# Kernel optimization log

Hardware: AMD Instinct MI355X
Metric: run time of the kernel (lower is better)

Reference implementation:

```python
import jax, jax.numpy as jnp
import numpy as np

B, NT, NC, EMB = 8, 512, 2048, 512
H, DK, DV = 8, 64, 64
EPS = 1e-6


def setup_inputs() -> dict:
    key = jax.random.key(0)
    ks = jax.random.split(key, 11)
    s = 1.0 / np.sqrt(EMB)
    return {
        "queries": jax.random.normal(ks[0], (B, NT, EMB), jnp.float32),
        "keys": jax.random.normal(ks[1], (B, NC, EMB), jnp.float32),
        "values": jax.random.normal(ks[2], (B, NC, EMB), jnp.float32),
        "W_At": jax.random.normal(ks[3], (H * DK, EMB), jnp.float32) * s,
        "b_At": jax.random.normal(ks[4], (H * DK,), jnp.float32) * s,
        "W_Ac": jax.random.normal(ks[5], (H * DK, EMB), jnp.float32) * s,
        "b_Ac": jax.random.normal(ks[6], (H * DK,), jnp.float32) * s,
        "W_Bc": jax.random.normal(ks[7], (H * DV, EMB), jnp.float32) * s,
        "b_Bc": jax.random.normal(ks[8], (H * DV,), jnp.float32) * s,
        "W_R": jax.random.normal(ks[9], (EMB, H * DV), jnp.float32) * (1.0 / np.sqrt(H * DV)),
        "b_R": jax.random.normal(ks[10], (EMB,), jnp.float32) * (1.0 / np.sqrt(H * DV)),
    }


def reference(queries, keys, values, W_At, b_At, W_Ac, b_Ac, W_Bc, b_Bc, W_R, b_R):
    b_s, n_t, _ = queries.shape
    n_c = keys.shape[1]
    # projections -> (b, h, n, d)
    q = (queries @ W_At.T + b_At).reshape(b_s, n_t, H, DK).transpose(0, 2, 1, 3)
    k = (keys @ W_Ac.T + b_Ac).reshape(b_s, n_c, H, DK).transpose(0, 2, 1, 3)
    v = (values @ W_Bc.T + b_Bc).reshape(b_s, n_c, H, DV).transpose(0, 2, 1, 3)
    # cosine similarity: q.k / max(||q||*||k||, eps) -- no (b,h,nt,nc,dk) broadcast
    dots = jnp.einsum("bhtd,bhcd->bhtc", q, k)
    qn = jnp.linalg.norm(q, axis=-1)  # (b,h,nt)
    kn = jnp.linalg.norm(k, axis=-1)  # (b,h,nc)
    denom = jnp.maximum(qn[..., :, None] * kn[..., None, :], EPS)
    att = jax.nn.softmax(dots / denom, axis=-1)
    out = jnp.einsum("bhtc,bhcd->bhtd", att, v)
    out = out.transpose(0, 2, 1, 3).reshape(b_s, n_t, H * DV)
    out = out @ W_R.T + b_R
    return (out, att)
```

## Files before the change

kernel.cpp:

```cpp
#include <hip/hip_runtime.h>

#define B_   8
#define NT_  512
#define NC_  2048
#define EMB_ 512
#define H_   8

typedef __attribute__((ext_vector_type(8))) short bf16x8;
typedef __attribute__((ext_vector_type(4))) float f32x4;

__device__ __forceinline__ unsigned short f2bf(float x) {
    unsigned u = __float_as_uint(x);
    u += 0x7fffu + ((u >> 16) & 1u);
    return (unsigned short)(u >> 16);
}
__device__ __forceinline__ float b2f(unsigned short h) {
    return __uint_as_float(((unsigned)h) << 16);
}

__device__ __forceinline__ int swz(int row, int col) {
    return row * 64 + ((((col >> 3) ^ row) & 7) << 3) + (col & 7);
}

__device__ __forceinline__ bf16x8 ldfrag(const unsigned short* t, int rowbase, int kq) {
    int lane = threadIdx.x & 63;
    int m = rowbase + (lane & 15);
    int k = kq + ((lane >> 4) << 3);
    return *(const bf16x8*)(t + swz(m, k));
}

template<int NCH>
__device__ __forceinline__ void stage_f32(unsigned short* tile, const float* src, int ld) {
    int tid = threadIdx.x;
#pragma unroll
    for (int i = 0; i < NCH; i++) {
        int ch  = tid + i * 256;
        int row = ch >> 3, c8 = ch & 7;
        const float4* p = (const float4*)(src + (size_t)row * ld + c8 * 8);
        float4 a = p[0], b = p[1];
        uint4 u;
        u.x = (unsigned)f2bf(a.x) | ((unsigned)f2bf(a.y) << 16);
        u.y = (unsigned)f2bf(a.z) | ((unsigned)f2bf(a.w) << 16);
        u.z = (unsigned)f2bf(b.x) | ((unsigned)f2bf(b.y) << 16);
        u.w = (unsigned)f2bf(b.z) | ((unsigned)f2bf(b.w) << 16);
        *(uint4*)(tile + row * 64 + (((c8 ^ row) & 7) << 3)) = u;
    }
}
template<int NCH>
__device__ __forceinline__ void stage_bf(unsigned short* tile, const unsigned short* src, int ld) {
    int tid = threadIdx.x;
#pragma unroll
    for (int i = 0; i < NCH; i++) {
        int ch  = tid + i * 256;
        int row = ch >> 3, c8 = ch & 7;
        uint4 u = *(const uint4*)(src + (size_t)row * ld + c8 * 8);
        *(uint4*)(tile + row * 64 + (((c8 ^ row) & 7) << 3)) = u;
    }
}

template<int MODE, bool ABF>
__global__ __launch_bounds__(256) void gemm512(const void* A, const float* W,
                                               const float* bias, void* dst, int sh)
{
    __shared__ unsigned short As[64 * 64];
    __shared__ unsigned short Bs[64 * 64];
    int r0 = blockIdx.x * 64;
    int n0 = blockIdx.y * 64;
    int tid = threadIdx.x;
    int w = tid >> 6, quad = (tid >> 4) & 3, l16 = tid & 15;
    f32x4 acc[4] = {};

    for (int k0 = 0; k0 < 512; k0 += 64) {
        __syncthreads();
        if (ABF) stage_bf<2>(As, (const unsigned short*)A + (size_t)r0 * 512 + k0, 512);
        else     stage_f32<2>(As, (const float*)A + (size_t)r0 * 512 + k0, 512);
        stage_f32<2>(Bs, W + (size_t)n0 * 512 + k0, 512);
        __syncthreads();
#pragma unroll
        for (int ks = 0; ks < 2; ks++) {
            bf16x8 af = ldfrag(As, 16 * w, 32 * ks);
#pragma unroll
            for (int nt = 0; nt < 4; nt++) {
                bf16x8 bfr = ldfrag(Bs, 16 * nt, 32 * ks);
                acc[nt] = __builtin_amdgcn_mfma_f32_16x16x32_bf16(af, bfr, acc[nt], 0, 0, 0);
            }
        }
    }

    float vals[4][4];
    float bn[4];
#pragma unroll
    for (int nt = 0; nt < 4; nt++) bn[nt] = bias[n0 + nt * 16 + l16];
#pragma unroll
    for (int nt = 0; nt < 4; nt++)
#pragma unroll
        for (int r = 0; r < 4; r++) vals[nt][r] = acc[nt][r] + bn[nt];

    if (MODE == 0) {
#pragma unroll
        for (int r = 0; r < 4; r++) {
            float ss = 0.f;
#pragma unroll
            for (int nt = 0; nt < 4; nt++) ss += vals[nt][r] * vals[nt][r];
#pragma unroll
            for (int m = 1; m <= 8; m <<= 1) ss += __shfl_xor(ss, m, 64);
            float sc = rsqrtf(fmaxf(ss, 1e-24f));
#pragma unroll
            for (int nt = 0; nt < 4; nt++) vals[nt][r] *= sc;
        }
    }

#pragma unroll
    for (int nt = 0; nt < 4; nt++) {
        int n = n0 + nt * 16 + l16;
        int h = n >> 6, d = n & 63;
#pragma unroll
        for (int r = 0; r < 4; r++) {
            int row = r0 + w * 16 + quad * 4 + r;
            float val = vals[nt][r];
            if (MODE == 0) {
                int b = row >> sh, nloc = row & ((1 << sh) - 1);
                ((unsigned short*)dst)[((((size_t)(b * H_ + h) << sh) + nloc) << 6) + d] = f2bf(val);
            } else if (MODE == 1) {
                int b = row >> sh, nloc = row & ((1 << sh) - 1);
                ((unsigned short*)dst)[(((size_t)((b * H_ + h) * 64 + d)) << sh) + nloc] = f2bf(val);
            } else {
                ((float*)dst)[(size_t)row * 512 + n] = val;
            }
        }
    }
}

#define SPAD 2056

__global__ __launch_bounds__(256) void attn_fused(const unsigned short* qh,
                                                  const unsigned short* kh,
                                                  const unsigned short* vt,
                                                  float* attout,
                                                  unsigned short* oh)
{
    __shared__ unsigned short Sp[32 * SPAD];
    __shared__ unsigned short Ks[128 * 64];
    __shared__ unsigned short Qs[32 * 64];
    __shared__ float invs[32];
    int bh = blockIdx.y;
    int t0 = blockIdx.x * 32;
    int tid = threadIdx.x;
    int w = tid >> 6, quad = (tid >> 4) & 3, l16 = tid & 15;

    stage_bf<1>(Qs, qh + ((size_t)bh * NT_ + t0) * 64, 64);
    __syncthreads();
    bf16x8 qf[2][2];
#pragma unroll
    for (int mt = 0; mt < 2; mt++)
#pragma unroll
        for (int ks = 0; ks < 2; ks++) qf[mt][ks] = ldfrag(Qs, 16 * mt, 32 * ks);

    for (int c0 = 0; c0 < NC_; c0 += 128) {
        __syncthreads();
        stage_bf<4>(Ks, kh + ((size_t)bh * NC_ + c0) * 64, 64);
        __syncthreads();
#pragma unroll
        for (int nt = 0; nt < 2; nt++) {
#pragma unroll
            for (int mt = 0; mt < 2; mt++) {
                f32x4 acc = {};
#pragma unroll
                for (int ks = 0; ks < 2; ks++) {
                    bf16x8 bfr = ldfrag(Ks, 32 * w + 16 * nt, 32 * ks);
                    acc = __builtin_amdgcn_mfma_f32_16x16x32_bf16(qf[mt][ks], bfr, acc, 0, 0, 0);
                }
                int c = c0 + 32 * w + 16 * nt + l16;
#pragma unroll
                for (int r = 0; r < 4; r++) {
                    int tr = 16 * mt + quad * 4 + r;
                    Sp[tr * SPAD + c] = f2bf(__expf(acc[r]));
                }
            }
        }
    }
    __syncthreads();

    {
        int r = tid >> 3, p = tid & 7;
        float s = 0.f;
#pragma unroll 4
        for (int i = 0; i < 32; i++) {
            uint4 u = *(const uint4*)(Sp + r * SPAD + p * 8 + 64 * i);
            s += b2f((unsigned short)(u.x)) + b2f((unsigned short)(u.x >> 16))
               + b2f((unsigned short)(u.y)) + b2f((unsigned short)(u.y >> 16))
               + b2f((unsigned short)(u.z)) + b2f((unsigned short)(u.z >> 16))
               + b2f((unsigned short)(u.w)) + b2f((unsigned short)(u.w >> 16));
        }
#pragma unroll
        for (int m = 1; m <= 4; m <<= 1) s += __shfl_xor(s, m, 64);
        if (p == 0) invs[r] = 1.0f / s;
    }
    __syncthreads();

    int wr_r = tid >> 3, wr_p = tid & 7;
    float inv_wr = invs[wr_r];
    float* attbase = attout + ((size_t)bh * NT_ + t0) * 2048;
    f32x4 oacc[2] = {};

    for (int c0 = 0; c0 < NC_; c0 += 64) {
        __syncthreads();
        stage_bf<2>(Ks, vt + (size_t)bh * 64 * NC_ + c0, NC_);
        __syncthreads();
#pragma unroll
        for (int ks = 0; ks < 2; ks++) {
            bf16x8 bfr = ldfrag(Ks, 16 * w, 32 * ks);
#pragma unroll
            for (int mt = 0; mt < 2; mt++) {
                bf16x8 af;
                {
                    int m = 16 * mt + (tid & 15);
                    int k = c0 + 32 * ks + (((tid >> 4) & 3) << 3);
                    af = *(const bf16x8*)(Sp + m * SPAD + k);
                }
                oacc[mt] = __builtin_amdgcn_mfma_f32_16x16x32_bf16(af, bfr, oacc[mt], 0, 0, 0);
            }
        }
        {
            uint4 u = *(const uint4*)(Sp + wr_r * SPAD + c0 + wr_p * 8);
            f32x4 f0, f1;
            f0.x = b2f((unsigned short)(u.x)) * inv_wr;
            f0.y = b2f((unsigned short)(u.x >> 16)) * inv_wr;
            f0.z = b2f((unsigned short)(u.y)) * inv_wr;
            f0.w = b2f((unsigned short)(u.y >> 16)) * inv_wr;
            f1.x = b2f((unsigned short)(u.z)) * inv_wr;
            f1.y = b2f((unsigned short)(u.z >> 16)) * inv_wr;
            f1.z = b2f((unsigned short)(u.w)) * inv_wr;
            f1.w = b2f((unsigned short)(u.w >> 16)) * inv_wr;
            f32x4* dstp = (f32x4*)(attbase + (size_t)wr_r * 2048 + c0 + wr_p * 8);
            __builtin_nontemporal_store(f0, dstp);
            __builtin_nontemporal_store(f1, dstp + 1);
        }
    }

    int b = bh >> 3, h = bh & 7;
    int d = 16 * w + l16;
#pragma unroll
    for (int mt = 0; mt < 2; mt++) {
#pragma unroll
        for (int r = 0; r < 4; r++) {
            int t = 16 * mt + quad * 4 + r;
            float val = oacc[mt][r] * invs[t];
            oh[(size_t)(b * NT_ + t0 + t) * 512 + h * 64 + d] = f2bf(val);
        }
    }
}

extern "C" void kernel_launch(void* const* d_in, const int* in_sizes, int n_in,
                              void* d_out, int out_size, void* d_ws, size_t ws_size,
                              hipStream_t stream)
{
    (void)in_sizes; (void)n_in; (void)out_size; (void)ws_size;
    const float* queries = (const float*)d_in[0];
    const float* keys    = (const float*)d_in[1];
    const float* values  = (const float*)d_in[2];
    const float* W_At    = (const float*)d_in[3];
    const float* b_At    = (const float*)d_in[4];
    const float* W_Ac    = (const float*)d_in[5];
    const float* b_Ac    = (const float*)d_in[6];
    const float* W_Bc    = (const float*)d_in[7];
    const float* b_Bc    = (const float*)d_in[8];
    const float* W_R     = (const float*)d_in[9];
    const float* b_R     = (const float*)d_in[10];

    float* out0   = (float*)d_out;
    float* attout = out0 + (size_t)B_ * NT_ * EMB_;

    unsigned short* ws = (unsigned short*)d_ws;
    unsigned short* qh = ws;
    unsigned short* kh = qh + (size_t)2097152;
    unsigned short* vt = kh + (size_t)8388608;
    unsigned short* oh = vt + (size_t)8388608;

    dim3 blk(256);

    gemm512<0, false><<<dim3(4096 / 64, 8),  blk, 0, stream>>>(queries, W_At, b_At, qh, 9);
    gemm512<0, false><<<dim3(16384 / 64, 8), blk, 0, stream>>>(keys,    W_Ac, b_Ac, kh, 11);
    gemm512<1, false><<<dim3(16384 / 64, 8), blk, 0, stream>>>(values,  W_Bc, b_Bc, vt, 11);

    attn_fused<<<dim3(NT_ / 32, B_ * H_), blk, 0, stream>>>(qh, kh, vt, attout, oh);

    gemm512<2, true><<<dim3(4096 / 64, 8), blk, 0, stream>>>(oh, W_R, b_R, out0, 0);
}
```

Baseline: 541.7 us.

## Replace LDS-resident score row with two-pass recompute attention kernel

Drops the 32x2048 bf16 score buffer held in shared memory (about 130KB per block). The first pass computes exp scores, accumulates row sums in registers and does the PV product tile by tile through a small swizzled P buffer. A second pass recomputes QK^T to write the normalized attention matrix directly to global memory. This shrinks LDS so several blocks can share a CU (launch_bounds 256,3), at the cost of doing QK^T twice, reloading K, and making the attention stores scattered 4-byte nontemporal writes instead of 16-byte vector stores.

Result: faster. 514.2 us (-5.1%).

```diff
diff --git a/kernel.cpp b/kernel.cpp
--- a/kernel.cpp
+++ b/kernel.cpp
@@ -131,122 +131,132 @@
     }
 }
 
-#define SPAD 2056
-
-__global__ __launch_bounds__(256) void attn_fused(const unsigned short* qh,
-                                                  const unsigned short* kh,
-                                                  const unsigned short* vt,
-                                                  float* attout,
-                                                  unsigned short* oh)
+__global__ __launch_bounds__(256, 3) void attn_fused(const unsigned short* qh,
+                                                     const unsigned short* kh,
+                                                     const unsigned short* vt,
+                                                     float* attout,
+                                                     unsigned short* oh)
 {
-    __shared__ unsigned short Sp[32 * SPAD];
     __shared__ unsigned short Ks[128 * 64];
-    __shared__ unsigned short Qs[32 * 64];
+    __shared__ unsigned short Vs[2][64 * 64];
+    __shared__ unsigned short Pt[2][32 * 64];
+    __shared__ float red[4][32];
     __shared__ float invs[32];
     int bh = blockIdx.y;
     int t0 = blockIdx.x * 32;
     int tid = threadIdx.x;
     int w = tid >> 6, quad = (tid >> 4) & 3, l16 = tid & 15;
 
-    stage_bf<1>(Qs, qh + ((size_t)bh * NT_ + t0) * 64, 64);
+    stage_bf<1>((unsigned short*)Pt, qh + ((size_t)bh * NT_ + t0) * 64, 64);
     __syncthreads();
     bf16x8 qf[2][2];
 #pragma unroll
     for (int mt = 0; mt < 2; mt++)
 #pragma unroll
-        for (int ks = 0; ks < 2; ks++) qf[mt][ks] = ldfrag(Qs, 16 * mt, 32 * ks);
+        for (int ks = 0; ks < 2; ks++) qf[mt][ks] = ldfrag((unsigned short*)Pt, 16 * mt, 32 * ks);
+
+    const unsigned short* kbase = kh + (size_t)bh * NC_ * 64;
+    const unsigned short* vbase = vt + (size_t)bh * 64 * NC_;
+
+    f32x4 oacc[2] = {};
+    float rs[2][4] = {};
 
     for (int c0 = 0; c0 < NC_; c0 += 128) {
         __syncthreads();
-        stage_bf<4>(Ks, kh + ((size_t)bh * NC_ + c0) * 64, 64);
+        stage_bf<4>(Ks, kbase + (size_t)c0 * 64, 64);
+        stage_bf<2>(Vs[0], vbase + c0, NC_);
+        stage_bf<2>(Vs[1], vbase + c0 + 64, NC_);
         __syncthreads();
 #pragma unroll
         for (int nt = 0; nt < 2; nt++) {
+            int cl = 32 * w + 16 * nt;
+            int half = cl >> 6, cc = cl & 63;
 #pragma unroll
             for (int mt = 0; mt < 2; mt++) {
                 f32x4 acc = {};
 #pragma unroll
                 for (int ks = 0; ks < 2; ks++) {
-                    bf16x8 bfr = ldfrag(Ks, 32 * w + 16 * nt, 32 * ks);
+                    bf16x8 bfr = ldfrag(Ks, cl, 32 * ks);
                     acc = __builtin_amdgcn_mfma_f32_16x16x32_bf16(qf[mt][ks], bfr, acc, 0, 0, 0);
                 }
-                int c = c0 + 32 * w + 16 * nt + l16;
 #pragma unroll
                 for (int r = 0; r < 4; r++) {
-                    int tr = 16 * mt + quad * 4 + r;
-                    Sp[tr * SPAD + c] = f2bf(__expf(acc[r]));
-                }
-            }
-        }
-    }
+                    int t = 16 * mt + quad * 4 + r;
+                    float p = __expf(acc[r]);
+                    rs[mt][r] += p;
+                    Pt[half][swz(t, cc + l16)] = f2bf(p);
+                }
+            }
+        }
+        __syncthreads();
+#pragma unroll
+        for (int half = 0; half < 2; half++) {
+#pragma unroll
+            for (int ks = 0; ks < 2; ks++) {
+                bf16x8 vfr = ldfrag(Vs[half], 16 * w, 32 * ks);
+#pragma unroll
+                for (int mt = 0; mt < 2; mt++) {
+                    bf16x8 af = ldfrag((unsigned short*)Pt[half], 16 * mt, 32 * ks);
+                    oacc[mt] = __builtin_amdgcn_mfma_f32_16x16x32_bf16(af, vfr, oacc[mt], 0, 0, 0);
+                }
+            }
+        }
+    }
+
+#pragma unroll
+    for (int mt = 0; mt < 2; mt++)
+#pragma unroll
+        for (int r = 0; r < 4; r++) {
+            float s = rs[mt][r];
+#pragma unroll
+            for (int m = 1; m <= 8; m <<= 1) s += __shfl_xor(s, m, 64);
+            if (l16 == 0) red[w][16 * mt + quad * 4 + r] = s;
+        }
     __syncthreads();
+    if (tid < 32) invs[tid] = 1.0f / (red[0][tid] + red[1][tid] + red[2][tid] + red[3][tid]);
+    __syncthreads();
 
     {
-        int r = tid >> 3, p = tid & 7;
-        float s = 0.f;
-#pragma unroll 4
-        for (int i = 0; i < 32; i++) {
-            uint4 u = *(const uint4*)(Sp + r * SPAD + p * 8 + 64 * i);
-            s += b2f((unsigned short)(u.x)) + b2f((unsigned short)(u.x >> 16))
-               + b2f((unsigned short)(u.y)) + b2f((unsigned short)(u.y >> 16))
-               + b2f((unsigned short)(u.z)) + b2f((unsigned short)(u.z >> 16))
-               + b2f((unsigned short)(u.w)) + b2f((unsigned short)(u.w >> 16));
-        }
-#pragma unroll
-        for (int m = 1; m <= 4; m <<= 1) s += __shfl_xor(s, m, 64);
-        if (p == 0) invs[r] = 1.0f / s;
-    }
-    __syncthreads();
-
-    int wr_r = tid >> 3, wr_p = tid & 7;
-    float inv_wr = invs[wr_r];
+        int b = bh >> 3, h = bh & 7;
+        int d = 16 * w + l16;
+#pragma unroll
+        for (int mt = 0; mt < 2; mt++)
+#pragma unroll
+            for (int r = 0; r < 4; r++) {
+                int t = 16 * mt + quad * 4 + r;
+                oh[(size_t)(b * NT_ + t0 + t) * 512 + h * 64 + d] = f2bf(oacc[mt][r] * invs[t]);
+            }
+    }
+
     float* attbase = attout + ((size_t)bh * NT_ + t0) * 2048;
-    f32x4 oacc[2] = {};
-
-    for (int c0 = 0; c0 < NC_; c0 += 64) {
-        __syncthreads();
-        stage_bf<2>(Ks, vt + (size_t)bh * 64 * NC_ + c0, NC_);
-        __syncthreads();
-#pragma unroll
-        for (int ks = 0; ks < 2; ks++) {
-            bf16x8 bfr = ldfrag(Ks, 16 * w, 32 * ks);
+    float myinv[2][4];
+#pragma unroll
+    for (int mt = 0; mt < 2; mt++)
+#pragma unroll
+        for (int r = 0; r < 4; r++) myinv[mt][r] = invs[16 * mt + quad * 4 + r];
+
+    for (int c0 = 0; c0 < NC_; c0 += 128) {
+        __syncthreads();
+        stage_bf<4>(Ks, kbase + (size_t)c0 * 64, 64);
+        __syncthreads();
+#pragma unroll
+        for (int nt = 0; nt < 2; nt++) {
+            int cl = 32 * w + 16 * nt;
 #pragma unroll
             for (int mt = 0; mt < 2; mt++) {
-                bf16x8 af;
-                {
-                    int m = 16 * mt + (tid & 15);
-                    int k = c0 + 32 * ks + (((tid >> 4) & 3) << 3);
-                    af = *(const bf16x8*)(Sp + m * SPAD + k);
-                }
-                oacc[mt] = __builtin_amdgcn_mfma_f32_16x16x32_bf16(af, bfr, oacc[mt], 0, 0, 0);
-            }
-        }
-        {
-            uint4 u = *(const uint4*)(Sp + wr_r * SPAD + c0 + wr_p * 8);
-            f32x4 f0, f1;
-            f0.x = b2f((unsigned short)(u.x)) * inv_wr;
-            f0.y = b2f((unsigned short)(u.x >> 16)) * inv_wr;
-            f0.z = b2f((unsigned short)(u.y)) * inv_wr;
-            f0.w = b2f((unsigned short)(u.y >> 16)) * inv_wr;
-            f1.x = b2f((unsigned short)(u.z)) * inv_wr;
-            f1.y = b2f((unsigned short)(u.z >> 16)) * inv_wr;
-            f1.z = b2f((unsigned short)(u.w)) * inv_wr;
-            f1.w = b2f((unsigned short)(u.w >> 16)) * inv_wr;
-            f32x4* dstp = (f32x4*)(attbase + (size_t)wr_r * 2048 + c0 + wr_p * 8);
-            __builtin_nontemporal_store(f0, dstp);
-            __builtin_nontemporal_store(f1, dstp + 1);
-        }
-    }
-
-    int b = bh >> 3, h = bh & 7;
-    int d = 16 * w + l16;
-#pragma unroll
-    for (int mt = 0; mt < 2; mt++) {
-#pragma unroll
-        for (int r = 0; r < 4; r++) {
-            int t = 16 * mt + quad * 4 + r;
-            float val = oacc[mt][r] * invs[t];
-            oh[(size_t)(b * NT_ + t0 + t) * 512 + h * 64 + d] = f2bf(val);
+                f32x4 acc = {};
+#pragma unroll
+                for (int ks = 0; ks < 2; ks++) {
+                    bf16x8 bfr = ldfrag(Ks, cl, 32 * ks);
+                    acc = __builtin_amdgcn_mfma_f32_16x16x32_bf16(qf[mt][ks], bfr, acc, 0, 0, 0);
+                }
+#pragma unroll
+                for (int r = 0; r < 4; r++) {
+                    int t = 16 * mt + quad * 4 + r;
+                    __builtin_nontemporal_store(__expf(acc[r]) * myinv[mt][r],
+                                                attbase + (size_t)t * 2048 + c0 + cl + l16);
+                }
+            }
         }
     }
 }
```
